# Kernel tuning notes

Hardware: AMD Instinct MI355X
Metric: run time of the kernel (lower is better)

The kernel has to match this reference:

```python
import jax, jax.numpy as jnp
import numpy as np


def _conv2d(x, w):
    # x: [B,Cin,H,W], w: [Cout,Cin,kh,kw], stride 1, SAME padding
    return jax.lax.conv_general_dilated(x, w, (1, 1), 'SAME',
                                        dimension_numbers=('NCHW', 'OIHW', 'NCHW'))


def _conv1d(x, w):
    # x: [B,Cin,L], w: [Cout,Cin,k], stride 1, SAME padding
    return jax.lax.conv_general_dilated(x, w, (1,), 'SAME',
                                        dimension_numbers=('NCH', 'OIH', 'NCH'))


def setup_inputs() -> dict:
    key = jax.random.key(0)
    ks = jax.random.split(key, 5)
    B, cin, cout, H, W = 8, 256, 256, 64, 64
    x = jax.random.normal(ks[0], (B, cin, H, W), dtype=jnp.float32)
    # Conv weights, small init ~ 1/sqrt(fan_in)
    w_qkv = jax.random.normal(ks[1], (3 * cout, cin, 3, 3), dtype=jnp.float32) * (1.0 / np.sqrt(cin * 9))
    w_mod = jax.random.normal(ks[2], (2 * cout, cout, 3), dtype=jnp.float32) * (1.0 / np.sqrt(cout * 3))
    w_res = jax.random.normal(ks[3], (cout, cin, 1, 1), dtype=jnp.float32) * (1.0 / np.sqrt(cin))
    w_gate = jax.random.normal(ks[4], (cout, cin + cout, 1, 1), dtype=jnp.float32) * (1.0 / np.sqrt(cin + cout))
    return {'x': x, 'w_qkv': w_qkv, 'w_mod': w_mod, 'w_res': w_res, 'w_gate': w_gate}


def reference(x, w_qkv, w_mod, w_res, w_gate):
    B, C, H, W = x.shape
    cout = w_res.shape[0]
    L = H * W
    # qkv projection, then split and flatten spatial dims
    qkv = _conv2d(x, w_qkv).reshape(B, 3, cout, L)  # [B,3,cout,L]
    q, k, v = qkv[:, 0], qkv[:, 1], qkv[:, 2]       # each [B,cout,L]
    # modulation from v along the spatial axis (Conv1d)
    mod = _conv1d(v, w_mod).reshape(B, 2, cout, L)
    qm, km = mod[:, 0], mod[:, 1]
    # negate-relu softmax modulated scores over spatial axis
    m_q = jax.nn.softmax(-jax.nn.relu(q * qm), axis=-1)  # [B,cout,L]
    m_k = jax.nn.softmax(-jax.nn.relu(k * km), axis=-1)  # [B,cout,L]
    scale = 1.0 / jnp.sqrt(jnp.asarray(C, dtype=x.dtype))
    m_attn = jax.nn.softmax(jnp.einsum('bcl,bdl->bcd', m_q, m_k) * scale, axis=-1)  # [B,cout,cout]
    y = jnp.einsum('bcd,bdl->bcl', m_attn, v).reshape(B, cout, H, W)
    # sigmoid-gated residual blend
    g = jax.nn.sigmoid(_conv2d(jnp.concatenate([y, x], axis=1), w_gate))
    return g * _conv2d(x, w_res) + (1.0 - g) * y
```

## Files before the change

### kernel.cpp

```cpp
#include <hip/hip_runtime.h>
#include <cstdint>

typedef unsigned short u16;
using bf16x8 = __attribute__((ext_vector_type(8))) short;
using f32x4  = __attribute__((ext_vector_type(4))) float;

struct alignas(16) V16 { uint32_t a, b, c, d; };
struct alignas(8)  U16x4 { u16 a, b, c, d; };
struct alignas(16) F4 { float x, y, z, w; };

__device__ __forceinline__ u16 f2bf(float f) {
  uint32_t u = __float_as_uint(f);
  u += 0x7fffu + ((u >> 16) & 1u);
  return (u16)(u >> 16);
}
__device__ __forceinline__ float bf2f(u16 h) {
  return __uint_as_float(((uint32_t)h) << 16);
}

#define GLOAD16(g, l) __builtin_amdgcn_global_load_lds(                         \
    (const __attribute__((address_space(1))) uint32_t*)(g),                     \
    (__attribute__((address_space(3))) uint32_t*)(l), 16, 0, 0)

template<int MODE, int MF, int FUSE = 0>
__global__ __launch_bounds__(512, 2) void gemmOv_bf16(
    const u16* __restrict__ A, const u16* __restrict__ B, u16* __restrict__ otr,
    int sA, int sB, int64_t bBatch, int trStride, int64_t trBatch, int MT,
    const u16* __restrict__ zpage,
    const u16* __restrict__ fq = nullptr, u16* __restrict__ eOut = nullptr,
    float* __restrict__ partS = nullptr)
{
  constexpr int NS = (MODE == 2) ? 36 : 12;
  constexpr int ASL = MF * 2048;
  constexpr int SLAB = ASL + 16384;
  __shared__ __align__(16) u16 lds[2 * SLAB];

  const int tid = threadIdx.x;
  const int q = gridDim.x >> 3;
  const int flat = (blockIdx.x & 7) * q + (blockIdx.x >> 3);
  const int per_b = MT * 16;
  const int b = flat / per_b, rem = flat % per_b;
  const int ntile = rem / MT, mtile = rem % MT;
  const int m0 = mtile * (MF * 32), n0 = ntile * 256;
  const u16* Bb = B + (int64_t)b * bBatch;

  const int lane = tid & 63, wave = tid >> 6;
  const int wm = wave >> 2, wn = wave & 3;
  const int lr = lane & 15, lc = lane >> 4;

  const int lrow8 = lane >> 3;
  const int sch  = lane & 7;
  const int scs  = sch ^ (lrow8 & 7);
  const u16* aSrc[MF / 2];
  const u16* bSrc[4];
  int bRow[4];
#pragma unroll
  for (int j = 0; j < MF / 2; ++j)
    aSrc[j] = A + (int64_t)(m0 + wave * (MF * 4) + j * 8 + lrow8) * sA + scs * 8;
#pragma unroll
  for (int j = 0; j < 4; ++j) {
    bRow[j] = n0 + wave * 32 + j * 8 + lrow8;
    bSrc[j] = Bb + (int64_t)bRow[j] * sB + scs * 8;
  }

  auto stageA = [&](int s) {
    const int kOff = (s >> 2) * 256 + ((s & 3) << 6);
    u16* dst = lds + (s & 1) * SLAB + wave * (MF / 2) * 512;
#pragma unroll
    for (int j = 0; j < MF / 2; ++j)
      GLOAD16(aSrc[j] + kOff, dst + j * 512);
  };
  auto stageB = [&](int s) {
    const int tap = s >> 2, kc = (s & 3) << 6;
    int off, dh = 0, dw = 0;
    if constexpr (MODE == 2) { dh = tap / 3 - 1; dw = tap % 3 - 1; off = dh * 64 + dw; }
    else                     { off = tap - 1; }
    u16* dst = lds + (s & 1) * SLAB + ASL + wave * 2048;
#pragma unroll
    for (int j = 0; j < 4; ++j) {
      bool ok;
      if constexpr (MODE == 2) {
        int hh = (bRow[j] >> 6) + dh, ww = (bRow[j] & 63) + dw;
        ok = ((unsigned)hh < 64u) && ((unsigned)ww < 64u);
      } else {
        ok = ((unsigned)(bRow[j] + off) < 4096u);
      }
      const u16* src = ok ? (bSrc[j] + (int64_t)off * sB + kc) : zpage;
      GLOAD16(src, dst + j * 512);
    }
  };

  f32x4 acc[MF][4];
#pragma unroll
  for (int i = 0; i < MF; ++i)
#pragma unroll
    for (int j = 0; j < 4; ++j) acc[i][j] = f32x4{0.f, 0.f, 0.f, 0.f};

  stageA(0); stageB(0);
  asm volatile("s_waitcnt vmcnt(0)" ::: "memory");
  __builtin_amdgcn_s_barrier();
  __builtin_amdgcn_sched_barrier(0);

  for (int s = 0; s < NS; ++s) {
    const u16* As = lds + (s & 1) * SLAB;
    const u16* Bs = As + ASL;
    const bool pf = (s + 1 < NS);
    bf16x8 bfr[4], af[MF];

#pragma unroll
    for (int nf = 0; nf < 4; ++nf) {
      int row = wn * 64 + nf * 16 + lr;
      bfr[nf] = *(const bf16x8*)&Bs[row * 64 + ((lc ^ (row & 7)) * 8)];
    }
#pragma unroll
    for (int mf = 0; mf < MF; ++mf) {
      int row = wm * (MF * 16) + mf * 16 + lr;
      af[mf] = *(const bf16x8*)&As[row * 64 + ((lc ^ (row & 7)) * 8)];
    }
    if (pf) stageA(s + 1);
    __builtin_amdgcn_s_setprio(1);
#pragma unroll
    for (int mf = 0; mf < MF; ++mf)
#pragma unroll
      for (int nf = 0; nf < 4; ++nf)
        acc[mf][nf] = __builtin_amdgcn_mfma_f32_16x16x32_bf16(af[mf], bfr[nf], acc[mf][nf], 0, 0, 0);
    __builtin_amdgcn_s_setprio(0);

#pragma unroll
    for (int nf = 0; nf < 4; ++nf) {
      int row = wn * 64 + nf * 16 + lr;
      bfr[nf] = *(const bf16x8*)&Bs[row * 64 + (((4 + lc) ^ (row & 7)) * 8)];
    }
#pragma unroll
    for (int mf = 0; mf < MF; ++mf) {
      int row = wm * (MF * 16) + mf * 16 + lr;
      af[mf] = *(const bf16x8*)&As[row * 64 + (((4 + lc) ^ (row & 7)) * 8)];
    }
    if (pf) stageB(s + 1);
    __builtin_amdgcn_s_setprio(1);
#pragma unroll
    for (int mf = 0; mf < MF; ++mf)
#pragma unroll
      for (int nf = 0; nf < 4; ++nf)
        acc[mf][nf] = __builtin_amdgcn_mfma_f32_16x16x32_bf16(af[mf], bfr[nf], acc[mf][nf], 0, 0, 0);
    __builtin_amdgcn_s_setprio(0);

    if (pf) {
      asm volatile("s_waitcnt vmcnt(0)" ::: "memory");
      __builtin_amdgcn_s_barrier();
      __builtin_amdgcn_sched_barrier(0);
    }
  }

  if constexpr (FUSE) {
    const u16* qk = fq + (int64_t)b * 4096 * 768;
    u16* eb = eOut + (int64_t)b * 512 * 4096;
    float* ps = partS + (int64_t)b * 512 * 64;
#pragma unroll
    for (int mf = 0; mf < MF; ++mf) {
      const int mbase = m0 + wm * (MF * 16) + mf * 16 + lc * 4;
      float sp[4] = {0.f, 0.f, 0.f, 0.f};
#pragma unroll
      for (int nf = 0; nf < 4; ++nf) {
        int n = n0 + wn * 64 + nf * 16 + lr;
        U16x4 qv = *(const U16x4*)(qk + (int64_t)n * 768 + mbase);
        const u16* qp = (const u16*)&qv;
        f32x4 v = acc[mf][nf];
#pragma unroll
        for (int r = 0; r < 4; ++r) {
          float z = bf2f(qp[r]) * v[r];
          float e = __expf(z > 0.f ? -z : 0.f);
          sp[r] += e;
          eb[(int64_t)(mbase + r) * 4096 + n] = f2bf(e);
        }
      }
#pragma unroll
      for (int r = 0; r < 4; ++r) {
        float sv = sp[r];
        sv += __shfl_xor(sv, 1);
        sv += __shfl_xor(sv, 2);
        sv += __shfl_xor(sv, 4);
        sv += __shfl_xor(sv, 8);
        if (lr == 0)
          ps[(int64_t)(mbase + r) * 64 + ntile * 4 + wn] = sv;
      }
    }
  } else {
#pragma unroll
    for (int mf = 0; mf < MF; ++mf)
#pragma unroll
      for (int nf = 0; nf < 4; ++nf) {
        f32x4 v = acc[mf][nf];
        int m = m0 + wm * (MF * 16) + mf * 16 + lc * 4;
        int n = n0 + wn * 64 + nf * 16 + lr;
        U16x4 pk{f2bf(v[0]), f2bf(v[1]), f2bf(v[2]), f2bf(v[3])};
        *(U16x4*)(otr + trBatch * b + (int64_t)n * trStride + m) = pk;
      }
  }
}

__global__ __launch_bounds__(256) void gemm_scores(
    const u16* __restrict__ A, const u16* __restrict__ B,
    float* __restrict__ orm,
    int sA, int64_t aBatch, int sB, int64_t bBatch,
    int rmStride, int64_t rmBatch,
    int nsplit, int kStep, int64_t splitOut)
{
  __shared__ __align__(16) u16 As[128 * 32];
  __shared__ __align__(16) u16 Bs[128 * 32];

  const int tid = threadIdx.x;
  int b = blockIdx.z, split = 0;
  if (nsplit > 1) { split = b % nsplit; b /= nsplit; }
  const int m0  = blockIdx.y * 128;
  const int n0  = blockIdx.x * 128;
  const int lane = tid & 63, wave = tid >> 6;
  const int wm = wave >> 1, wn = wave & 1;
  const int lr = lane & 15, lc = lane >> 4;

  f32x4 acc[4][4];
#pragma unroll
  for (int i = 0; i < 4; ++i)
#pragma unroll
    for (int j = 0; j < 4; ++j) acc[i][j] = f32x4{0.f, 0.f, 0.f, 0.f};

  const u16* Ab = A + (int64_t)b * aBatch + split * kStep;
  const u16* Bb = B + (int64_t)b * bBatch + split * kStep;

  const int srow = tid >> 2;
  const int sc   = tid & 3;
  const int scs  = sc ^ (srow & 3);

  for (int kc = 0; kc < 512; kc += 32) {
#pragma unroll
    for (int it = 0; it < 2; ++it) {
      int row = srow + it * 64;
      GLOAD16(Ab + (int64_t)(m0 + row) * sA + kc + scs * 8,
              &As[wave * 512 + it * 2048]);
      GLOAD16(Bb + (int64_t)(n0 + row) * sB + kc + scs * 8,
              &Bs[wave * 512 + it * 2048]);
    }
    __syncthreads();

    bf16x8 af[4], bfr[4];
#pragma unroll
    for (int mf = 0; mf < 4; ++mf) {
      int row = wm * 64 + mf * 16 + lr;
      af[mf] = *(const bf16x8*)&As[row * 32 + ((lc ^ (row & 3)) * 8)];
    }
#pragma unroll
    for (int nf = 0; nf < 4; ++nf) {
      int row = wn * 64 + nf * 16 + lr;
      bfr[nf] = *(const bf16x8*)&Bs[row * 32 + ((lc ^ (row & 3)) * 8)];
    }
#pragma unroll
    for (int mf = 0; mf < 4; ++mf)
#pragma unroll
      for (int nf = 0; nf < 4; ++nf)
        acc[mf][nf] = __builtin_amdgcn_mfma_f32_16x16x32_bf16(af[mf], bfr[nf], acc[mf][nf], 0, 0, 0);
    __syncthreads();
  }

#pragma unroll
  for (int mf = 0; mf < 4; ++mf)
#pragma unroll
    for (int nf = 0; nf < 4; ++nf) {
      f32x4 v = acc[mf][nf];
      int m = m0 + wm * 64 + mf * 16 + lc * 4;
      int n = n0 + wn * 64 + nf * 16 + lr;
      float* p = orm + splitOut * split + rmBatch * b + (int64_t)m * rmStride + n;
#pragma unroll
      for (int r = 0; r < 4; ++r) p[(int64_t)r * rmStride] = v[r];
    }
}

__global__ __launch_bounds__(512) void k_tail(
    const u16* __restrict__ mattn, const u16* __restrict__ qkvT,
    const u16* __restrict__ ycatT, const u16* __restrict__ Wg,
    const u16* __restrict__ Wr, float* __restrict__ out)
{
  __shared__ __align__(16) u16 As[256 * 32];
  __shared__ __align__(16) u16 As2[256 * 32];
  __shared__ __align__(16) u16 Bs[128 * 32];
  __shared__ __align__(16) u16 yT[128 * 260];

  const int b = blockIdx.y, l0 = blockIdx.x * 128;
  const int tid = threadIdx.x;
  const int lane = tid & 63, wave = tid >> 6;
  const int wm = wave >> 1, wn = wave & 1;
  const int lr = lane & 15, lc = lane >> 4;

  const int srow = tid >> 2, sc = tid & 3;
  const int scs = sc ^ (srow & 3);

  f32x4 acc[4][4];
#pragma unroll
  for (int i = 0; i < 4; ++i)
#pragma unroll
    for (int j = 0; j < 4; ++j) acc[i][j] = f32x4{0.f, 0.f, 0.f, 0.f};

  const u16* Am = mattn + (int64_t)b * 65536;
  const u16* Vv = qkvT + (int64_t)b * 4096 * 768 + 512;
  for (int kc = 0; kc < 256; kc += 32) {
#pragma unroll
    for (int it = 0; it < 2; ++it) {
      int row = srow + it * 128;
      GLOAD16(Am + (int64_t)row * 256 + kc + scs * 8,
              &As[wave * 512 + it * 4096]);
    }
    GLOAD16(Vv + (int64_t)(l0 + srow) * 768 + kc + scs * 8, &Bs[wave * 512]);
    __syncthreads();

    bf16x8 af[4], bfr[4];
#pragma unroll
    for (int mf = 0; mf < 4; ++mf) {
      int row = wm * 64 + mf * 16 + lr;
      af[mf] = *(const bf16x8*)&As[row * 32 + ((lc ^ (row & 3)) * 8)];
    }
#pragma unroll
    for (int nf = 0; nf < 4; ++nf) {
      int row = wn * 64 + nf * 16 + lr;
      bfr[nf] = *(const bf16x8*)&Bs[row * 32 + ((lc ^ (row & 3)) * 8)];
    }
#pragma unroll
    for (int mf = 0; mf < 4; ++mf)
#pragma unroll
      for (int nf = 0; nf < 4; ++nf)
        acc[mf][nf] = __builtin_amdgcn_mfma_f32_16x16x32_bf16(af[mf], bfr[nf], acc[mf][nf], 0, 0, 0);
    __syncthreads();
  }

#pragma unroll
  for (int mf = 0; mf < 4; ++mf)
#pragma unroll
    for (int nf = 0; nf < 4; ++nf) {
      f32x4 v = acc[mf][nf];
      int m = wm * 64 + mf * 16 + lc * 4;
      int n = wn * 64 + nf * 16 + lr;
      U16x4 pk{f2bf(v[0]), f2bf(v[1]), f2bf(v[2]), f2bf(v[3])};
      *(U16x4*)&yT[n * 260 + m] = pk;
    }
  __syncthreads();

  f32x4 acc2[4][4];
#pragma unroll
  for (int i = 0; i < 4; ++i)
#pragma unroll
    for (int j = 0; j < 4; ++j) {
      acc[i][j] = f32x4{0.f, 0.f, 0.f, 0.f};
      acc2[i][j] = f32x4{0.f, 0.f, 0.f, 0.f};
    }

  const u16* Xc = ycatT + (int64_t)b * 4096 * 512;
  for (int kc = 0; kc < 512; kc += 32) {
    const bool xk = (kc >= 256);
#pragma unroll
    for (int it = 0; it < 2; ++it) {
      int row = srow + it * 128;
      GLOAD16(Wg + (int64_t)row * 512 + kc + scs * 8,
              &As[wave * 512 + it * 4096]);
    }
    if (xk) {
#pragma unroll
      for (int it = 0; it < 2; ++it) {
        int row = srow + it * 128;
        GLOAD16(Wr + (int64_t)row * 256 + (kc - 256) + scs * 8,
                &As2[wave * 512 + it * 4096]);
      }
      GLOAD16(Xc + (int64_t)(l0 + srow) * 512 + kc + scs * 8, &Bs[wave * 512]);
    }
    __syncthreads();

    bf16x8 af[4], bfr[4];
#pragma unroll
    for (int nf = 0; nf < 4; ++nf) {
      int row = wn * 64 + nf * 16 + lr;
      if (xk) bfr[nf] = *(const bf16x8*)&Bs[row * 32 + ((lc ^ (row & 3)) * 8)];
      else    bfr[nf] = *(const bf16x8*)&yT[row * 260 + kc + lc * 8];
    }
#pragma unroll
    for (int mf = 0; mf < 4; ++mf) {
      int row = wm * 64 + mf * 16 + lr;
      af[mf] = *(const bf16x8*)&As[row * 32 + ((lc ^ (row & 3)) * 8)];
    }
#pragma unroll
    for (int mf = 0; mf < 4; ++mf)
#pragma unroll
      for (int nf = 0; nf < 4; ++nf)
        acc[mf][nf] = __builtin_amdgcn_mfma_f32_16x16x32_bf16(af[mf], bfr[nf], acc[mf][nf], 0, 0, 0);
    if (xk) {
      bf16x8 af2[4];
#pragma unroll
      for (int mf = 0; mf < 4; ++mf) {
        int row = wm * 64 + mf * 16 + lr;
        af2[mf] = *(const bf16x8*)&As2[row * 32 + ((lc ^ (row & 3)) * 8)];
      }
#pragma unroll
      for (int mf = 0; mf < 4; ++mf)
#pragma unroll
        for (int nf = 0; nf < 4; ++nf)
          acc2[mf][nf] = __builtin_amdgcn_mfma_f32_16x16x32_bf16(af2[mf], bfr[nf], acc2[mf][nf], 0, 0, 0);
    }
    __syncthreads();
  }

#pragma unroll
  for (int mf = 0; mf < 4; ++mf)
#pragma unroll
    for (int nf = 0; nf < 4; ++nf) {
      f32x4 g4 = acc[mf][nf], r4 = acc2[mf][nf];
      int m = wm * 64 + mf * 16 + lc * 4;
      int n = wn * 64 + nf * 16 + lr;
      U16x4 yv = *(const U16x4*)&yT[n * 260 + m];
      const u16* yp = (const u16*)&yv;
      float* p = out + (int64_t)b * 256 * 4096 + (int64_t)m * 4096 + l0 + n;
#pragma unroll
      for (int r = 0; r < 4; ++r) {
        float g = 1.f / (1.f + __expf(-g4[r]));
        p[(int64_t)r * 4096] = g * r4[r] + (1.f - g) * bf2f(yp[r]);
      }
    }
}

__global__ void k_prep(const float* __restrict__ wqkv, const float* __restrict__ wmod,
                       const float* __restrict__ wgate, const float* __restrict__ wres,
                       u16* __restrict__ Wa, u16* __restrict__ Wb,
                       u16* __restrict__ Wg, u16* __restrict__ Wr,
                       uint32_t* __restrict__ zpage) {
  int bid = blockIdx.x, t = threadIdx.x;
  if (bid < 6912) {
    int idx = bid * 256 + t;
    if (idx < 768 * 2304) {
      int oc = idx / 2304, r = idx % 2304;
      int tap = r >> 8, ic = r & 255;
      Wa[idx] = f2bf(wqkv[((oc * 256 + ic) * 3 + tap / 3) * 3 + tap % 3]);
    }
  } else if (bid < 8448) {
    int idx = (bid - 6912) * 256 + t;
    if (idx < 512 * 768) {
      int oc = idx / 768, r = idx % 768;
      int tap = r >> 8, ic = r & 255;
      Wb[idx] = f2bf(wmod[(oc * 256 + ic) * 3 + tap]);
    }
  } else if (bid < 8960) {
    int idx = (bid - 8448) * 256 + t;
    if (idx < 131072) Wg[idx] = f2bf(wgate[idx]);
  } else if (bid < 9216) {
    int idx = (bid - 8960) * 256 + t;
    if (idx < 65536) Wr[idx] = f2bf(wres[idx]);
  } else {
    if (t < 64) zpage[t] = 0u;
  }
}

__global__ __launch_bounds__(256) void k_xT(const float* __restrict__ x, u16* __restrict__ ycat) {
  __shared__ float tile[64 * 68];
  int b = blockIdx.z, c0 = blockIdx.y * 64, l0 = blockIdx.x * 64;
  int t = threadIdx.x;
  int cc = t >> 2, part = t & 3;
  const float* xp = x + ((int64_t)(b * 256 + c0 + cc)) * 4096 + l0 + part * 16;
#pragma unroll
  for (int j = 0; j < 4; ++j) {
    F4 v = *(const F4*)(xp + j * 4);
    float* tp = &tile[cc * 68 + part * 16 + j * 4];
    tp[0] = v.x; tp[1] = v.y; tp[2] = v.z; tp[3] = v.w;
  }
  __syncthreads();
  int l = t >> 2;
  u16* op = ycat + ((int64_t)b * 4096 + l0 + l) * 512 + 256 + c0 + part * 16;
  __align__(16) u16 tmp[16];
#pragma unroll
  for (int j = 0; j < 16; ++j) tmp[j] = f2bf(tile[(part * 16 + j) * 68 + l]);
  *(V16*)(op) = *(V16*)&tmp[0];
  *(V16*)(op + 8) = *(V16*)&tmp[8];
}

__global__ void k_statsB64(const float* __restrict__ part, float* __restrict__ inv) {
  int idx = blockIdx.x * 256 + threadIdx.x;
  float S = 0.f;
#pragma unroll
  for (int s = 0; s < 64; ++s) S += part[(int64_t)idx * 64 + s];
  inv[idx] = 1.0f / S;
}

__global__ __launch_bounds__(256) void k_softmax_attn(
    const float* __restrict__ sc, const float* __restrict__ invS,
    u16* __restrict__ ma, int nsplit, int64_t splitOff) {
  int c = blockIdx.x, b = blockIdx.y;
  int64_t base = ((int64_t)b * 256 + c) * 256;
  int t = threadIdx.x;
  float z = 0.f;
  for (int s = 0; s < nsplit; ++s) z += sc[(int64_t)s * splitOff + base + t];
  float iq = invS[(int64_t)b * 512 + c];
  float ik = invS[(int64_t)b * 512 + 256 + t];
  z *= iq * ik * 0.0625f;
  __shared__ float red[256];
  red[t] = z; __syncthreads();
  for (int s = 128; s > 0; s >>= 1) { if (t < s) red[t] = fmaxf(red[t], red[t + s]); __syncthreads(); }
  float M = red[0]; __syncthreads();
  float p = __expf(z - M);
  red[t] = p; __syncthreads();
  for (int s = 128; s > 0; s >>= 1) { if (t < s) red[t] += red[t + s]; __syncthreads(); }
  ma[base + t] = f2bf(p / red[0]);
}

extern "C" void kernel_launch(void* const* d_in, const int* in_sizes, int n_in,
                              void* d_out, int out_size, void* d_ws, size_t ws_size,
                              hipStream_t stream) {
  (void)in_sizes; (void)n_in; (void)out_size; (void)ws_size;
  const float* x      = (const float*)d_in[0];
  const float* w_qkv  = (const float*)d_in[1];
  const float* w_mod  = (const float*)d_in[2];
  const float* w_res  = (const float*)d_in[3];
  const float* w_gate = (const float*)d_in[4];
  float* out = (float*)d_out;

  char* p = (char*)d_ws;
  auto take = [&](size_t n) { void* r = (void*)p; p += (n + 255) & ~(size_t)255; return r; };
  u16*    zpage  = (u16*)take(256);
  u16*    qkvT   = (u16*)take(50331648);
  u16*    ycatT  = (u16*)take(33554432);
  u16*    eT     = (u16*)take(33554432);
  float*  scores = (float*)take(16777216);
  u16*    mattn  = (u16*)take(1048576);
  float*  partS  = (float*)take(1048576);
  float*  invS   = (float*)take(16384);
  u16*    Wa     = (u16*)take(3538944);
  u16*    Wb     = (u16*)take(786432);
  u16*    Wg     = (u16*)take(262144);
  u16*    Wr     = (u16*)take(131072);

  k_prep<<<9217, 256, 0, stream>>>(w_qkv, w_mod, w_gate, w_res,
                                   Wa, Wb, Wg, Wr, (uint32_t*)zpage);
  k_xT<<<dim3(64, 4, 8), 256, 0, stream>>>(x, ycatT);

  gemmOv_bf16<2, 6><<<512, 512, 0, stream>>>(
      Wa, ycatT + 256, qkvT,
      2304, 512, (int64_t)4096 * 512,
      768, (int64_t)4096 * 768, 4, zpage);

  gemmOv_bf16<1, 8, 1><<<256, 512, 0, stream>>>(
      Wb, qkvT + 512, nullptr,
      768, 768, (int64_t)4096 * 768,
      0, 0, 2, zpage,
      qkvT, eT, partS);

  k_statsB64<<<16, 256, 0, stream>>>(partS, invS);

  gemm_scores<<<dim3(2, 2, 64), 256, 0, stream>>>(
      eT, eT + (int64_t)256 * 4096, scores,
      4096, (int64_t)512 * 4096,
      4096, (int64_t)512 * 4096,
      256, (int64_t)256 * 256,
      8, 512, (int64_t)8 * 256 * 256);

  k_softmax_attn<<<dim3(256, 8), 256, 0, stream>>>(
      scores, invS, mattn, 8, (int64_t)8 * 256 * 256);

  k_tail<<<dim3(32, 8), 512, 0, stream>>>(mattn, qkvT, ycatT, Wg, Wr, out);
}
```

Before: 218.3 us.

## Use smaller 192x128 tile GEMM kernel with 256 threads for QKV conv

Adds a new implicit-GEMM kernel for the 3x3 QKV convolution that uses 256-thread blocks with 192x128 output tiles, a two-slab double-buffered LDS pipeline, and staggered A/B prefetch between MFMA halves. The launch switches from 512 blocks of 512 threads to 1024 blocks of 256 threads. The goal is better occupancy and load balance across CUs and less LDS per block. The cost is lower per-block data reuse and more total tiles to schedule.

```diff
diff --git a/kernel.cpp b/kernel.cpp
--- a/kernel.cpp
+++ b/kernel.cpp
@@ -21,6 +21,147 @@
 #define GLOAD16(g, l) __builtin_amdgcn_global_load_lds(                         \
     (const __attribute__((address_space(1))) uint32_t*)(g),                     \
     (__attribute__((address_space(3))) uint32_t*)(l), 16, 0, 0)
+
+template<int MODE>
+__global__ __launch_bounds__(256, 2) void gemm2b_bf16(
+    const u16* __restrict__ A, const u16* __restrict__ B, u16* __restrict__ otr,
+    int sA, int sB, int64_t bBatch, int trStride, int64_t trBatch, int MT,
+    const u16* __restrict__ zpage)
+{
+  constexpr int NS = (MODE == 2) ? 36 : 12;
+  constexpr int ASL = 12288;
+  constexpr int BSL = 8192;
+  constexpr int SLAB = ASL + BSL;
+  __shared__ __align__(16) u16 lds[2 * SLAB];
+
+  const int tid = threadIdx.x;
+  const int q = gridDim.x >> 3;
+  const int flat = (blockIdx.x & 7) * q + (blockIdx.x >> 3);
+  const int per_b = MT * 32;
+  const int b = flat / per_b, rem = flat % per_b;
+  const int ntile = rem / MT, mtile = rem % MT;
+  const int m0 = mtile * 192, n0 = ntile * 128;
+  const u16* Bb = B + (int64_t)b * bBatch;
+
+  const int lane = tid & 63, wave = tid >> 6;
+  const int wm = wave >> 1, wn = wave & 1;
+  const int lr = lane & 15, lc = lane >> 4;
+
+  const int srow = tid >> 3;
+  const int sch  = lane & 7;
+  const int scs  = sch ^ (srow & 7);
+  const u16* aSrc[6];
+  const u16* bSrc[4];
+  int bRow[4];
+#pragma unroll
+  for (int j = 0; j < 6; ++j)
+    aSrc[j] = A + (int64_t)(m0 + srow + j * 32) * sA + scs * 8;
+#pragma unroll
+  for (int j = 0; j < 4; ++j) {
+    bRow[j] = n0 + srow + j * 32;
+    bSrc[j] = Bb + (int64_t)bRow[j] * sB + scs * 8;
+  }
+
+  auto stageA = [&](int s) {
+    const int kOff = (s >> 2) * 256 + ((s & 3) << 6);
+    u16* dst = lds + (s & 1) * SLAB + wave * 512;
+#pragma unroll
+    for (int j = 0; j < 6; ++j)
+      GLOAD16(aSrc[j] + kOff, dst + j * 2048);
+  };
+  auto stageB = [&](int s) {
+    const int tap = s >> 2, kc = (s & 3) << 6;
+    int off, dh = 0, dw = 0;
+    if constexpr (MODE == 2) { dh = tap / 3 - 1; dw = tap % 3 - 1; off = dh * 64 + dw; }
+    else                     { off = tap - 1; }
+    u16* dst = lds + (s & 1) * SLAB + ASL + wave * 512;
+#pragma unroll
+    for (int j = 0; j < 4; ++j) {
+      bool ok;
+      if constexpr (MODE == 2) {
+        int hh = (bRow[j] >> 6) + dh, ww = (bRow[j] & 63) + dw;
+        ok = ((unsigned)hh < 64u) && ((unsigned)ww < 64u);
+      } else {
+        ok = ((unsigned)(bRow[j] + off) < 4096u);
+      }
+      const u16* src = ok ? (bSrc[j] + (int64_t)off * sB + kc) : zpage;
+      GLOAD16(src, dst + j * 2048);
+    }
+  };
+
+  f32x4 acc[6][4];
+#pragma unroll
+  for (int i = 0; i < 6; ++i)
+#pragma unroll
+    for (int j = 0; j < 4; ++j) acc[i][j] = f32x4{0.f, 0.f, 0.f, 0.f};
+
+  stageA(0); stageB(0); stageA(1); stageB(1);
+  asm volatile("s_waitcnt vmcnt(10)" ::: "memory");
+  __builtin_amdgcn_s_barrier();
+  __builtin_amdgcn_sched_barrier(0);
+
+  for (int s = 0; s < NS; ++s) {
+    const u16* As = lds + (s & 1) * SLAB;
+    const u16* Bs = As + ASL;
+    const bool pf = (s + 1 < NS);
+    bf16x8 bfr[4], af[6];
+
+#pragma unroll
+    for (int nf = 0; nf < 4; ++nf) {
+      int row = wn * 64 + nf * 16 + lr;
+      bfr[nf] = *(const bf16x8*)&Bs[row * 64 + ((lc ^ (row & 7)) * 8)];
+    }
+#pragma unroll
+    for (int mf = 0; mf < 6; ++mf) {
+      int row = wm * 96 + mf * 16 + lr;
+      af[mf] = *(const bf16x8*)&As[row * 64 + ((lc ^ (row & 7)) * 8)];
+    }
+    if (pf) stageA(s + 1);
+    __builtin_amdgcn_s_setprio(1);
+#pragma unroll
+    for (int mf = 0; mf < 6; ++mf)
+#pragma unroll
+      for (int nf = 0; nf < 4; ++nf)
+        acc[mf][nf] = __builtin_amdgcn_mfma_f32_16x16x32_bf16(af[mf], bfr[nf], acc[mf][nf], 0, 0, 0);
+    __builtin_amdgcn_s_setprio(0);
+
+#pragma unroll
+    for (int nf = 0; nf < 4; ++nf) {
+      int row = wn * 64 + nf * 16 + lr;
+      bfr[nf] = *(const bf16x8*)&Bs[row * 64 + (((4 + lc) ^ (row & 7)) * 8)];
+    }
+#pragma unroll
+    for (int mf = 0; mf < 6; ++mf) {
+      int row = wm * 96 + mf * 16 + lr;
+      af[mf] = *(const bf16x8*)&As[row * 64 + (((4 + lc) ^ (row & 7)) * 8)];
+    }
+    if (pf) stageB(s + 1);
+    __builtin_amdgcn_s_setprio(1);
+#pragma unroll
+    for (int mf = 0; mf < 6; ++mf)
+#pragma unroll
+      for (int nf = 0; nf < 4; ++nf)
+        acc[mf][nf] = __builtin_amdgcn_mfma_f32_16x16x32_bf16(af[mf], bfr[nf], acc[mf][nf], 0, 0, 0);
+    __builtin_amdgcn_s_setprio(0);
+
+    if (pf) {
+      asm volatile("s_waitcnt vmcnt(0)" ::: "memory");
+      __builtin_amdgcn_s_barrier();
+      __builtin_amdgcn_sched_barrier(0);
+    }
+  }
+
+#pragma unroll
+  for (int mf = 0; mf < 6; ++mf)
+#pragma unroll
+    for (int nf = 0; nf < 4; ++nf) {
+      f32x4 v = acc[mf][nf];
+      int m = m0 + wm * 96 + mf * 16 + lc * 4;
+      int n = n0 + wn * 64 + nf * 16 + lr;
+      U16x4 pk{f2bf(v[0]), f2bf(v[1]), f2bf(v[2]), f2bf(v[3])};
+      *(U16x4*)(otr + trBatch * b + (int64_t)n * trStride + m) = pk;
+    }
+}
 
 template<int MODE, int MF, int FUSE = 0>
 __global__ __launch_bounds__(512, 2) void gemmOv_bf16(
@@ -534,7 +675,7 @@
                                    Wa, Wb, Wg, Wr, (uint32_t*)zpage);
   k_xT<<<dim3(64, 4, 8), 256, 0, stream>>>(x, ycatT);
 
-  gemmOv_bf16<2, 6><<<512, 512, 0, stream>>>(
+  gemm2b_bf16<2><<<1024, 256, 0, stream>>>(
       Wa, ycatT + 256, qkvT,
       2304, 512, (int64_t)4096 * 512,
       768, (int64_t)4096 * 768, 4, zpage);
```

New measurement: 223.9 us. 2.5% more time.
